# Optimization experiments

Measured on AMD Instinct MI355X. Metric: run time of the kernel, lower is better.

## Reference

```python
import jax, jax.numpy as jnp
import numpy as np

N_NODES = 100000
N_EDGES = 3200000
N_FEAT = 128
N_HID = 64


def gcn_conv(x, src, dst, ew, W, b, n):
    # x: [N, Fin]; src/dst: [E'] incl. self-loops; ew: [E'] edge weights
    xw = x @ W  # [N, Fout]
    deg = jax.ops.segment_sum(ew, dst, num_segments=n)  # [N]
    dinv = jnp.where(deg > 0, jax.lax.rsqrt(jnp.maximum(deg, 1e-12)), 0.0)
    norm = dinv[src] * ew * dinv[dst]  # [E']
    out = jax.ops.segment_sum(norm[:, None] * xw[src], dst, num_segments=n)
    return out + b


def setup_inputs() -> dict:
    key = jax.random.key(0)
    k = jax.random.split(key, 8)
    x = jax.random.normal(k[0], (N_NODES, N_FEAT), dtype=jnp.float32)
    edge_index = jax.random.randint(k[1], (2, N_EDGES), 0, N_NODES, dtype=jnp.int32)
    edge_attr = jax.random.uniform(k[2], (N_EDGES,), dtype=jnp.float32)
    s1 = 1.0 / np.sqrt(N_FEAT)
    s2 = 1.0 / np.sqrt(N_HID)
    W1 = jax.random.uniform(k[3], (N_FEAT, N_HID), minval=-s1, maxval=s1, dtype=jnp.float32)
    b1 = jnp.zeros((N_HID,), dtype=jnp.float32)
    W2 = jax.random.uniform(k[4], (N_HID, 1), minval=-s2, maxval=s2, dtype=jnp.float32)
    b2 = jnp.zeros((1,), dtype=jnp.float32)
    return {"x": x, "edge_index": edge_index, "edge_attr": edge_attr,
            "W1": W1, "b1": b1, "W2": W2, "b2": b2}


def reference(x, edge_index, edge_attr, W1, b1, W2, b2):
    n = x.shape[0]
    # add self-loops with weight 1 (PyG gcn_norm, improved=False)
    loop = jnp.arange(n, dtype=edge_index.dtype)
    src = jnp.concatenate([edge_index[0], loop])
    dst = jnp.concatenate([edge_index[1], loop])
    ew = jnp.concatenate([edge_attr, jnp.ones((n,), dtype=edge_attr.dtype)])
    h = gcn_conv(x, src, dst, ew, W1, b1, n)
    h = jax.nn.relu(h)
    # dropout is identity in eval mode
    out = gcn_conv(h, src, dst, ew, W2, b2, n)
    return out
```

## Files before the change

### kernel.cpp

```cpp
#include <hip/hip_runtime.h>
#include <hip/hip_fp16.h>


#define NPB_LOG 8
#define NPB     256
#define PCAP    8832
#define NEDG    4096

typedef _Float16 f16x8 __attribute__((ext_vector_type(8)));
typedef float    f32x4 __attribute__((ext_vector_type(4)));

__global__ void k_initcur(int* __restrict__ gcur, int npart) {
    int i = blockIdx.x * blockDim.x + threadIdx.x;
    if (i < npart) gcur[i] = i * PCAP;
}

__global__ __launch_bounds__(256) void k_binA(const int* __restrict__ src,
                                              const int* __restrict__ dst,
                                              const float* __restrict__ ea,
                                              int* __restrict__ gcur,
                                              uint2* __restrict__ part,
                                              int E, int npart) {
    __shared__ uint2 stag[NEDG];
    __shared__ unsigned short stagb[NEDG];
    __shared__ int hist[512];
    __shared__ int lofs[512];
    __shared__ int base[512];
    __shared__ int tsum[256];
    int t = threadIdx.x;
    int c0 = blockIdx.x * NEDG;
    hist[t] = 0; hist[t + 256] = 0;
    __syncthreads();
    for (int j = t; j < NEDG; j += 256) {
        int e = c0 + j;
        if (e < E) atomicAdd(&hist[dst[e] >> NPB_LOG], 1);
    }
    __syncthreads();
    int h0 = hist[2 * t], h1 = hist[2 * t + 1];
    int s = h0 + h1;
    tsum[t] = s;
    __syncthreads();
    for (int off = 1; off < 256; off <<= 1) {
        int u = (t >= off) ? tsum[t - off] : 0;
        __syncthreads();
        tsum[t] += u;
        __syncthreads();
    }
    int texcl = tsum[t] - s;
    lofs[2 * t]     = texcl;
    lofs[2 * t + 1] = texcl + h0;
    __syncthreads();
    for (int b = t; b < npart; b += 256) {
        int v = hist[b];
        if (v > 0) base[b] = atomicAdd(&gcur[b], v);
    }
    __syncthreads();
    for (int b = t; b < 512; b += 256) hist[b] = lofs[b];
    __syncthreads();
    for (int j = t; j < NEDG; j += 256) {
        int e = c0 + j;
        if (e < E) {
            int d = dst[e];
            int b = d >> NPB_LOG;
            int p = atomicAdd(&hist[b], 1);
            stag[p]  = make_uint2((uint)src[e] | ((uint)(d & (NPB - 1)) << 17),
                                  __float_as_uint(ea[e]));
            stagb[p] = (unsigned short)b;
        }
    }
    __syncthreads();
    int nvalid = min(NEDG, E - c0);
    for (int j = t; j < nvalid; j += 256) {
        int b = stagb[j];
        int gp = base[b] + (j - lofs[b]);
        if (gp < (b + 1) * PCAP) part[gp] = stag[j];
    }
}

__global__ __launch_bounds__(256) void k_binB(const int* __restrict__ gcur,
                                              const uint2* __restrict__ part,
                                              int2* __restrict__ ecsr,
                                              int2* __restrict__ rowdesc,
                                              float* __restrict__ dinv, int n) {
    __shared__ int   cnt[NPB];
    __shared__ float wsum[NPB];
    __shared__ int   cur[NPB];
    __shared__ int   wsums[4];
    int b = blockIdx.x;
    int t = threadIdx.x;
    int lane = t & 63, wv = t >> 6;
    cnt[t] = 0; wsum[t] = 0.0f;
    __syncthreads();
    int beg = b * PCAP;
    int len = gcur[b] - beg;
    if (len > PCAP) len = PCAP;
    for (int j = t; j < len; j += NPB) {
        uint2 ed = part[beg + j];
        int dlow = (ed.x >> 17) & (NPB - 1);
        atomicAdd(&cnt[dlow], 1);
        atomicAdd(&wsum[dlow], __uint_as_float(ed.y));
    }
    __syncthreads();
    int v = cnt[t];
    int s = v;
    for (int off = 1; off < 64; off <<= 1) {
        int u = __shfl_up(s, off, 64);
        if (lane >= off) s += u;
    }
    if (lane == 63) wsums[wv] = s;
    __syncthreads();
    int wbase = 0;
    for (int k = 0; k < wv; ++k) wbase += wsums[k];
    int excl = s - v + wbase;
    cur[t] = excl;
    int node = (b << NPB_LOG) + t;
    if (node < n) {
        rowdesc[node] = make_int2(beg + excl, v);
        dinv[node]    = rsqrtf(1.0f + wsum[t]);
    }
    __syncthreads();
    for (int j = t; j < len; j += NPB) {
        uint2 ed = part[beg + j];
        int dlow = (ed.x >> 17) & (NPB - 1);
        int p = atomicAdd(&cur[dlow], 1);
        ecsr[beg + p] = make_int2((int)(ed.x & 0x1FFFF), (int)ed.y);
    }
}

#define XPAD 136
__global__ __launch_bounds__(256) void k_gemm1m(const float* __restrict__ x,
                                                const float* __restrict__ W1,
                                                const float* __restrict__ dinv,
                                                __half* __restrict__ xw2, int n) {
    __shared__ __align__(16) _Float16 xs[64 * XPAD];
    __shared__ __align__(16) _Float16 wt[64 * XPAD];
    int tid = threadIdx.x;
    int row0 = blockIdx.x * 64;
    for (int i = tid; i < 64 * 32; i += 256) {
        int r = i >> 5, k4 = i & 31;
        float4 f = make_float4(0.f, 0.f, 0.f, 0.f);
        int gr = row0 + r;
        if (gr < n) f = ((const float4*)x)[(size_t)gr * 32 + k4];
        union { _Float16 h[4]; uint2 u; } tmp;
        tmp.h[0] = (_Float16)f.x; tmp.h[1] = (_Float16)f.y;
        tmp.h[2] = (_Float16)f.z; tmp.h[3] = (_Float16)f.w;
        *(uint2*)&xs[r * XPAD + k4 * 4] = tmp.u;
    }
    for (int i = tid; i < 128 * 64; i += 256) {
        int k = i >> 6, nn = i & 63;
        wt[nn * XPAD + k] = (_Float16)W1[i];
    }
    __syncthreads();

    int strip = tid >> 6;
    int lane  = tid & 63;
    int quad  = lane >> 4;
    int m     = lane & 15;
    f32x4 acc[4] = {{0,0,0,0},{0,0,0,0},{0,0,0,0},{0,0,0,0}};
#pragma unroll
    for (int kc = 0; kc < 4; ++kc) {
        f16x8 a = *(const f16x8*)&xs[(strip * 16 + m) * XPAD + kc * 32 + quad * 8];
#pragma unroll
        for (int nt = 0; nt < 4; ++nt) {
            f16x8 b = *(const f16x8*)&wt[(nt * 16 + m) * XPAD + kc * 32 + quad * 8];
            acc[nt] = __builtin_amdgcn_mfma_f32_16x16x32_f16(a, b, acc[nt], 0, 0, 0);
        }
    }
    float dv[4];
#pragma unroll
    for (int reg = 0; reg < 4; ++reg) {
        int gr = row0 + strip * 16 + quad * 4 + reg;
        dv[reg] = (gr < n) ? dinv[gr] : 0.0f;
    }
#pragma unroll
    for (int nt = 0; nt < 4; ++nt) {
#pragma unroll
        for (int reg = 0; reg < 4; ++reg) {
            int gr = row0 + strip * 16 + quad * 4 + reg;
            if (gr < n)
                xw2[(size_t)gr * 64 + nt * 16 + m] = __float2half(dv[reg] * acc[nt][reg]);
        }
    }
}

__global__ __launch_bounds__(256) void k_agg1f(const int2* __restrict__ rowdesc,
                                               const int2* __restrict__ ecsr,
                                               const float* __restrict__ dinv,
                                               const __half* __restrict__ xw2,
                                               const float* __restrict__ b1,
                                               const float* __restrict__ W2,
                                               float* __restrict__ g, int n) {
    int i = blockIdx.x * 4 + (threadIdx.x >> 6);
    int lane = threadIdx.x & 63;
    if (i >= n) return;
    int2 rd = rowdesc[i];
    int beg = __builtin_amdgcn_readfirstlane(rd.x);
    int len = __builtin_amdgcn_readfirstlane(rd.y);
    const int2* __restrict__ ep = ecsr + beg;

    float a0 = __half2float(xw2[(size_t)i * 64 + lane]);
    float a1 = 0.0f, a2 = 0.0f, a3 = 0.0f;
    int j = 0;
    for (; j + 8 <= len; j += 8) {
        int2 e0 = ep[j + 0];
        int2 e1 = ep[j + 1];
        int2 e2 = ep[j + 2];
        int2 e3 = ep[j + 3];
        int2 e4 = ep[j + 4];
        int2 e5 = ep[j + 5];
        int2 e6 = ep[j + 6];
        int2 e7 = ep[j + 7];
        float v0 = __half2float(xw2[(size_t)(uint)e0.x * 64 + lane]);
        float v1 = __half2float(xw2[(size_t)(uint)e1.x * 64 + lane]);
        float v2 = __half2float(xw2[(size_t)(uint)e2.x * 64 + lane]);
        float v3 = __half2float(xw2[(size_t)(uint)e3.x * 64 + lane]);
        float v4 = __half2float(xw2[(size_t)(uint)e4.x * 64 + lane]);
        float v5 = __half2float(xw2[(size_t)(uint)e5.x * 64 + lane]);
        float v6 = __half2float(xw2[(size_t)(uint)e6.x * 64 + lane]);
        float v7 = __half2float(xw2[(size_t)(uint)e7.x * 64 + lane]);
        a0 += __int_as_float(e0.y) * v0;
        a1 += __int_as_float(e1.y) * v1;
        a2 += __int_as_float(e2.y) * v2;
        a3 += __int_as_float(e3.y) * v3;
        a0 += __int_as_float(e4.y) * v4;
        a1 += __int_as_float(e5.y) * v5;
        a2 += __int_as_float(e6.y) * v6;
        a3 += __int_as_float(e7.y) * v7;
    }
    for (; j < len; ++j) {
        int2 e = ep[j];
        a0 += __int_as_float(e.y) * __half2float(xw2[(size_t)(uint)e.x * 64 + lane]);
    }
    float acc = (a0 + a1) + (a2 + a3);
    float di = dinv[i];
    float h = fmaxf(di * acc + b1[lane], 0.0f) * W2[lane];
    for (int off = 32; off; off >>= 1) h += __shfl_down(h, off, 64);
    if (lane == 0) g[i] = di * h;
}

__global__ __launch_bounds__(256) void k_agg2(const int2* __restrict__ rowdesc,
                                              const int2* __restrict__ ecsr,
                                              const float* __restrict__ dinv,
                                              const float* __restrict__ g,
                                              const float* __restrict__ b2,
                                              float* __restrict__ out, int n) {
    int i = blockIdx.x * 4 + (threadIdx.x >> 6);
    int lane = threadIdx.x & 63;
    if (i >= n) return;
    int2 rd = rowdesc[i];
    int beg = __builtin_amdgcn_readfirstlane(rd.x);
    int len = __builtin_amdgcn_readfirstlane(rd.y);
    const int2* __restrict__ ep = ecsr + beg;
    float p = 0.0f;
    for (int j = lane; j < len; j += 64) {
        int2 ed = ep[j];
        p += __int_as_float(ed.y) * g[ed.x];
    }
    for (int off = 32; off; off >>= 1) p += __shfl_down(p, off, 64);
    if (lane == 0) out[i] = b2[0] + dinv[i] * (g[i] + p);
}

extern "C" void kernel_launch(void* const* d_in, const int* in_sizes, int n_in,
                              void* d_out, int out_size, void* d_ws, size_t ws_size,
                              hipStream_t stream) {
    const float* x  = (const float*)d_in[0];
    const int*   ei = (const int*)  d_in[1];
    const float* ea = (const float*)d_in[2];
    const float* W1 = (const float*)d_in[3];
    const float* b1 = (const float*)d_in[4];
    const float* W2 = (const float*)d_in[5];
    const float* b2 = (const float*)d_in[6];
    float* out = (float*)d_out;

    int n = in_sizes[0] / 128;
    int E = in_sizes[1] / 2;
    const int* src = ei;
    const int* dst = ei + E;
    int npart = (n + NPB - 1) >> NPB_LOG;

    int*    ws       = (int*)d_ws;
    int*    gcur     = ws;
    uint2*  part     = (uint2*)(ws + 512);
    __half* xw2      = (__half*)part;
    size_t  psz      = (size_t)npart * PCAP;
    int2*   ecsr     = (int2*)(ws + 512 + psz * 2);
    int2*   rowdesc  = (int2*)(ws + 512 + psz * 4);
    float*  dinv     = (float*)(ws + 512 + psz * 4 + (size_t)2 * n);
    float*  g        = dinv + n;

    k_initcur<<<(npart + 255) / 256, 256, 0, stream>>>(gcur, npart);
    k_binA  <<<(E + NEDG - 1) / NEDG, 256, 0, stream>>>(src, dst, ea, gcur, part, E, npart);
    k_binB  <<<npart, NPB, 0, stream>>>(gcur, part, ecsr, rowdesc, dinv, n);
    k_gemm1m<<<(n + 63) / 64, 256, 0, stream>>>(x, W1, dinv, xw2, n);
    k_agg1f <<<(n + 3) / 4, 256, 0, stream>>>(rowdesc, ecsr, dinv, xw2, b1, W2, g, n);
    k_agg2  <<<(n + 3) / 4, 256, 0, stream>>>(rowdesc, ecsr, dinv, g, b2, out, n);
}
```

Measured before the change: 335.8 us.

## Replace two-pass partitioned binning with global-atomic degree count and scatter CSR build

Replaces the shared-memory partition binning (binA/binB with fixed-capacity partitions) with a simpler CSR build. A global-atomic degree and weight-sum pass feeds a per-wave scan with atomic base allocation, followed by an atomic-cursor scatter of edges. This removes the staging buffer and the partition capacity cap, but relies on millions of scattered global atomics with poor locality. Row ordering within the CSR becomes non-deterministic, and row bases are allocated in arbitrary wave order, which is still correct.

```diff
diff --git a/kernel.cpp b/kernel.cpp
--- a/kernel.cpp
+++ b/kernel.cpp
@@ -2,128 +2,64 @@
 #include <hip/hip_fp16.h>
 
 
-#define NPB_LOG 8
-#define NPB     256
-#define PCAP    8832
-#define NEDG    4096
-
 typedef _Float16 f16x8 __attribute__((ext_vector_type(8)));
 typedef float    f32x4 __attribute__((ext_vector_type(4)));
 
-__global__ void k_initcur(int* __restrict__ gcur, int npart) {
+__global__ __launch_bounds__(256) void k_zero(int* __restrict__ deg,
+                                              float* __restrict__ wsum,
+                                              int* __restrict__ gtot, int n) {
     int i = blockIdx.x * blockDim.x + threadIdx.x;
-    if (i < npart) gcur[i] = i * PCAP;
-}
-
-__global__ __launch_bounds__(256) void k_binA(const int* __restrict__ src,
-                                              const int* __restrict__ dst,
-                                              const float* __restrict__ ea,
-                                              int* __restrict__ gcur,
-                                              uint2* __restrict__ part,
-                                              int E, int npart) {
-    __shared__ uint2 stag[NEDG];
-    __shared__ unsigned short stagb[NEDG];
-    __shared__ int hist[512];
-    __shared__ int lofs[512];
-    __shared__ int base[512];
-    __shared__ int tsum[256];
-    int t = threadIdx.x;
-    int c0 = blockIdx.x * NEDG;
-    hist[t] = 0; hist[t + 256] = 0;
-    __syncthreads();
-    for (int j = t; j < NEDG; j += 256) {
-        int e = c0 + j;
-        if (e < E) atomicAdd(&hist[dst[e] >> NPB_LOG], 1);
-    }
-    __syncthreads();
-    int h0 = hist[2 * t], h1 = hist[2 * t + 1];
-    int s = h0 + h1;
-    tsum[t] = s;
-    __syncthreads();
-    for (int off = 1; off < 256; off <<= 1) {
-        int u = (t >= off) ? tsum[t - off] : 0;
-        __syncthreads();
-        tsum[t] += u;
-        __syncthreads();
-    }
-    int texcl = tsum[t] - s;
-    lofs[2 * t]     = texcl;
-    lofs[2 * t + 1] = texcl + h0;
-    __syncthreads();
-    for (int b = t; b < npart; b += 256) {
-        int v = hist[b];
-        if (v > 0) base[b] = atomicAdd(&gcur[b], v);
-    }
-    __syncthreads();
-    for (int b = t; b < 512; b += 256) hist[b] = lofs[b];
-    __syncthreads();
-    for (int j = t; j < NEDG; j += 256) {
-        int e = c0 + j;
-        if (e < E) {
-            int d = dst[e];
-            int b = d >> NPB_LOG;
-            int p = atomicAdd(&hist[b], 1);
-            stag[p]  = make_uint2((uint)src[e] | ((uint)(d & (NPB - 1)) << 17),
-                                  __float_as_uint(ea[e]));
-            stagb[p] = (unsigned short)b;
-        }
-    }
-    __syncthreads();
-    int nvalid = min(NEDG, E - c0);
-    for (int j = t; j < nvalid; j += 256) {
-        int b = stagb[j];
-        int gp = base[b] + (j - lofs[b]);
-        if (gp < (b + 1) * PCAP) part[gp] = stag[j];
-    }
-}
-
-__global__ __launch_bounds__(256) void k_binB(const int* __restrict__ gcur,
-                                              const uint2* __restrict__ part,
-                                              int2* __restrict__ ecsr,
+    if (i < n) { deg[i] = 0; wsum[i] = 0.0f; }
+    if (i == 0) *gtot = 0;
+}
+
+__global__ __launch_bounds__(256) void k_deg(const int* __restrict__ dst,
+                                             const float* __restrict__ ea,
+                                             int* __restrict__ deg,
+                                             float* __restrict__ wsum, int E) {
+    int stride = gridDim.x * blockDim.x;
+    for (int e = blockIdx.x * blockDim.x + threadIdx.x; e < E; e += stride) {
+        int d = dst[e];
+        atomicAdd(&deg[d], 1);
+        atomicAdd(&wsum[d], ea[e]);
+    }
+}
+
+__global__ __launch_bounds__(256) void k_rows(const int* __restrict__ deg,
+                                              const float* __restrict__ wsum,
+                                              int* __restrict__ gtot,
                                               int2* __restrict__ rowdesc,
+                                              int* __restrict__ cur,
                                               float* __restrict__ dinv, int n) {
-    __shared__ int   cnt[NPB];
-    __shared__ float wsum[NPB];
-    __shared__ int   cur[NPB];
-    __shared__ int   wsums[4];
-    int b = blockIdx.x;
-    int t = threadIdx.x;
-    int lane = t & 63, wv = t >> 6;
-    cnt[t] = 0; wsum[t] = 0.0f;
-    __syncthreads();
-    int beg = b * PCAP;
-    int len = gcur[b] - beg;
-    if (len > PCAP) len = PCAP;
-    for (int j = t; j < len; j += NPB) {
-        uint2 ed = part[beg + j];
-        int dlow = (ed.x >> 17) & (NPB - 1);
-        atomicAdd(&cnt[dlow], 1);
-        atomicAdd(&wsum[dlow], __uint_as_float(ed.y));
-    }
-    __syncthreads();
-    int v = cnt[t];
+    int i = blockIdx.x * blockDim.x + threadIdx.x;
+    int lane = threadIdx.x & 63;
+    int v = (i < n) ? deg[i] : 0;
     int s = v;
     for (int off = 1; off < 64; off <<= 1) {
         int u = __shfl_up(s, off, 64);
         if (lane >= off) s += u;
     }
-    if (lane == 63) wsums[wv] = s;
-    __syncthreads();
-    int wbase = 0;
-    for (int k = 0; k < wv; ++k) wbase += wsums[k];
-    int excl = s - v + wbase;
-    cur[t] = excl;
-    int node = (b << NPB_LOG) + t;
-    if (node < n) {
-        rowdesc[node] = make_int2(beg + excl, v);
-        dinv[node]    = rsqrtf(1.0f + wsum[t]);
-    }
-    __syncthreads();
-    for (int j = t; j < len; j += NPB) {
-        uint2 ed = part[beg + j];
-        int dlow = (ed.x >> 17) & (NPB - 1);
-        int p = atomicAdd(&cur[dlow], 1);
-        ecsr[beg + p] = make_int2((int)(ed.x & 0x1FFFF), (int)ed.y);
+    int tot = __shfl(s, 63, 64);
+    int base = 0;
+    if (lane == 0) base = atomicAdd(gtot, tot);
+    base = __shfl(base, 0, 64);
+    if (i < n) {
+        int rs = base + s - v;
+        rowdesc[i] = make_int2(rs, v);
+        cur[i]     = rs;
+        dinv[i]    = rsqrtf(1.0f + wsum[i]);
+    }
+}
+
+__global__ __launch_bounds__(256) void k_scatter(const int* __restrict__ src,
+                                                 const int* __restrict__ dst,
+                                                 const float* __restrict__ ea,
+                                                 int* __restrict__ cur,
+                                                 int2* __restrict__ ecsr, int E) {
+    int stride = gridDim.x * blockDim.x;
+    for (int e = blockIdx.x * blockDim.x + threadIdx.x; e < E; e += stride) {
+        int p = atomicAdd(&cur[dst[e]], 1);
+        ecsr[p] = make_int2(src[e], __float_as_int(ea[e]));
     }
 }
 
@@ -276,22 +212,26 @@
     int E = in_sizes[1] / 2;
     const int* src = ei;
     const int* dst = ei + E;
-    int npart = (n + NPB - 1) >> NPB_LOG;
 
     int*    ws       = (int*)d_ws;
-    int*    gcur     = ws;
-    uint2*  part     = (uint2*)(ws + 512);
-    __half* xw2      = (__half*)part;
-    size_t  psz      = (size_t)npart * PCAP;
-    int2*   ecsr     = (int2*)(ws + 512 + psz * 2);
-    int2*   rowdesc  = (int2*)(ws + 512 + psz * 4);
-    float*  dinv     = (float*)(ws + 512 + psz * 4 + (size_t)2 * n);
+    int*    gtot     = ws;
+    int*    deg      = ws + 256;
+    int*    cur      = deg + n;
+    float*  wsum     = (float*)(cur + n);
+    int2*   rowdesc  = (int2*)(wsum + n);
+    float*  dinv     = (float*)(rowdesc + n);
     float*  g        = dinv + n;
-
-    k_initcur<<<(npart + 255) / 256, 256, 0, stream>>>(gcur, npart);
-    k_binA  <<<(E + NEDG - 1) / NEDG, 256, 0, stream>>>(src, dst, ea, gcur, part, E, npart);
-    k_binB  <<<npart, NPB, 0, stream>>>(gcur, part, ecsr, rowdesc, dinv, n);
-    k_gemm1m<<<(n + 63) / 64, 256, 0, stream>>>(x, W1, dinv, xw2, n);
-    k_agg1f <<<(n + 3) / 4, 256, 0, stream>>>(rowdesc, ecsr, dinv, xw2, b1, W2, g, n);
-    k_agg2  <<<(n + 3) / 4, 256, 0, stream>>>(rowdesc, ecsr, dinv, g, b2, out, n);
-}
+    int2*   ecsr     = (int2*)(g + n);
+    __half* xw2      = (__half*)(ecsr + E);
+
+    int nb  = (n + 255) / 256;
+    int ebg = 2048;
+
+    k_zero   <<<nb, 256, 0, stream>>>(deg, wsum, gtot, n);
+    k_deg    <<<ebg, 256, 0, stream>>>(dst, ea, deg, wsum, E);
+    k_rows   <<<nb, 256, 0, stream>>>(deg, wsum, gtot, rowdesc, cur, dinv, n);
+    k_scatter<<<ebg, 256, 0, stream>>>(src, dst, ea, cur, ecsr, E);
+    k_gemm1m <<<(n + 63) / 64, 256, 0, stream>>>(x, W1, dinv, xw2, n);
+    k_agg1f  <<<(n + 3) / 4, 256, 0, stream>>>(rowdesc, ecsr, dinv, xw2, b1, W2, g, n);
+    k_agg2   <<<(n + 3) / 4, 256, 0, stream>>>(rowdesc, ecsr, dinv, g, b2, out, n);
+}
```

After: 802.2 us. 2.39x slower.
